# Kernel optimization log

Measured on AMD Instinct MI355X. Metric: run time of the kernel, lower is better.

Reference implementation:

```python
import jax, jax.numpy as jnp
import numpy as np

N = 8192
IN_F = 128
OUT_F = 64
ALPHA = 0.2  # LeakyReLU negative slope
EDGE_P = 0.02  # adjacency density
NEG_INF = -1e12


def setup_inputs() -> dict:
    key = jax.random.key(0)
    k1, k2, k3, k4 = jax.random.split(key, 4)
    input_h = jax.random.normal(k1, (N, IN_F), dtype=jnp.float32)
    # sparse-ish 0/1 adjacency mask, with self-loops so every softmax row is valid
    adj = (jax.random.uniform(k2, (N, N)) < EDGE_P).astype(jnp.float32)
    adj = adj + jnp.eye(N, dtype=jnp.float32)
    # xavier_uniform with gain 1.414 as in the torch init
    def xavier(k, shape, gain=1.414):
        fan_in, fan_out = shape[0], shape[1]
        bound = gain * np.sqrt(6.0 / (fan_in + fan_out))
        return jax.random.uniform(k, shape, jnp.float32, -bound, bound)
    W = xavier(k3, (IN_F, OUT_F))
    a = xavier(k4, (2 * OUT_F, 1))
    return {"input_h": input_h, "adj": adj, "W": W, "a": a}


def reference(input_h, adj, W, a):
    # Wh: [N, F]
    Wh = input_h @ W
    # e[i, j] = leakyrelu(a1 . Wh_i + a2 . Wh_j)  (decomposed, no N*N*2F concat)
    a1 = a[:OUT_F, 0]   # [F]
    a2 = a[OUT_F:, 0]   # [F]
    s_src = Wh @ a1     # [N]
    s_dst = Wh @ a2     # [N]
    e = jax.nn.leaky_relu(s_src[:, None] + s_dst[None, :], negative_slope=ALPHA)  # [N, N]
    att = jnp.where(adj > 0, e, NEG_INF)
    att = jax.nn.softmax(att, axis=1)
    # dropout is identity in eval mode (training=False)
    out_h = att @ Wh    # [N, F]
    return out_h
```

## Files before the change

### kernel.cpp

```cpp
#include <hip/hip_runtime.h>
#include <hip/hip_bf16.h>

#define N 8192
#define IN_F 128
#define OUT_F 64
#define ALPHA 0.2f
#define LOG2E 1.442695040888963f

typedef __attribute__((ext_vector_type(8))) short short8;
typedef __attribute__((ext_vector_type(4))) float f32x4;

__device__ __forceinline__ float cvt(float x) { return x; }
__device__ __forceinline__ float cvt(__hip_bfloat16 x) { return __bfloat162float(x); }

__device__ __forceinline__ bool probe_fp32(const void* adj) {
    unsigned int u = *(const unsigned int*)adj;
    return (u == 0x3F800000u) || (u == 0x40000000u);
}

__device__ __forceinline__ short f2bf(float x) {
    union { __hip_bfloat16 b; short s; } u;
    u.b = __float2bfloat16(x);
    return u.s;
}
__device__ __forceinline__ float bfbits2f(short s) {
    union { unsigned int u; float f; } v;
    v.u = ((unsigned int)(unsigned short)s) << 16;
    return v.f;
}

template <typename T>
__device__ __forceinline__ void k1_body(
    const T* __restrict__ h, const T* __restrict__ W, const T* __restrict__ a,
    unsigned short* __restrict__ WhT, float* __restrict__ s_src, float* __restrict__ s_dst,
    float (*WfT)[132], float (*hrow)[IN_F])
{
    const int tid  = threadIdx.x;
    const int w    = tid >> 6;
    const int lane = tid & 63;
    const int R0   = blockIdx.x * 16;

    for (int idx = tid; idx < IN_F * OUT_F; idx += 256) {
        int t = idx >> 6, f = idx & 63;
        WfT[f][t] = cvt(W[idx]);
    }
    for (int idx = tid; idx < 16 * IN_F; idx += 256) {
        int r = idx >> 7, c = idx & 127;
        hrow[r][c] = cvt(h[(size_t)(R0 + r) * IN_F + c]);
    }
    __syncthreads();

    const float a1 = cvt(a[lane]);
    const float a2 = cvt(a[OUT_F + lane]);

    for (int rr = 0; rr < 4; ++rr) {
        const int rloc = w * 4 + rr;
        const int i    = R0 + rloc;
        float acc = 0.f;
        #pragma unroll 8
        for (int b = 0; b < 32; ++b) {
            const float4 wv = *(const float4*)&WfT[lane][b * 4];
            const float4 hv = *(const float4*)&hrow[rloc][b * 4];
            acc = fmaf(hv.x, wv.x, acc);
            acc = fmaf(hv.y, wv.y, acc);
            acc = fmaf(hv.z, wv.z, acc);
            acc = fmaf(hv.w, wv.w, acc);
        }
        WhT[(size_t)lane * N + i] = (unsigned short)f2bf(acc);

        float s1 = acc * a1, s2 = acc * a2;
        #pragma unroll
        for (int off = 32; off; off >>= 1) {
            s1 += __shfl_xor(s1, off, 64);
            s2 += __shfl_xor(s2, off, 64);
        }
        if (lane == 0) { s_src[i] = s1; s_dst[i] = s2; }
    }
}

__global__ __launch_bounds__(256) void gat_k1(
    const void* h, const void* W, const void* a, const void* adj,
    unsigned short* WhT, float* s_src, float* s_dst)
{
    __shared__ float WfT[OUT_F][132];
    __shared__ float hrow[16][IN_F];
    if (probe_fp32(adj))
        k1_body<float>((const float*)h, (const float*)W, (const float*)a,
                       WhT, s_src, s_dst, WfT, hrow);
    else
        k1_body<__hip_bfloat16>((const __hip_bfloat16*)h, (const __hip_bfloat16*)W,
                                (const __hip_bfloat16*)a, WhT, s_src, s_dst, WfT, hrow);
}

#define K2_WAVES 8
template <typename TADJ, bool OUT_F32>
__device__ __forceinline__ void k2_body(
    const TADJ* __restrict__ adj,
    const unsigned short* __restrict__ WhT,
    const float* __restrict__ s_src,
    const float* __restrict__ s_dst,
    void* __restrict__ outv,
    float (*Cpart)[16][65], float (*Lpart)[16])
{
    const int tid  = threadIdx.x;
    const int wave = tid >> 6;
    const int lane = tid & 63;
    const int quad = lane >> 4;
    const int l15  = lane & 15;
    const int R0   = blockIdx.x * 16;

    const int   row = R0 + l15;
    const float si  = s_src[row];
    const TADJ* __restrict__ arow = adj + (size_t)row * N;

    f32x4 acc[4];
    #pragma unroll
    for (int nt = 0; nt < 4; ++nt) acc[nt] = (f32x4)0.f;
    float ls = 0.f;

    const int jw = wave * 1024;

    for (int kt = 0; kt < 32; ++kt) {
        const int jq = jw + kt * 32 + quad * 8;

        unsigned int bits[8];
        if constexpr (sizeof(TADJ) == 4) {
            const uint4 b0 = *(const uint4*)(arow + jq);
            const uint4 b1 = *(const uint4*)(arow + jq + 4);
            bits[0] = b0.x; bits[1] = b0.y; bits[2] = b0.z; bits[3] = b0.w;
            bits[4] = b1.x; bits[5] = b1.y; bits[6] = b1.z; bits[7] = b1.w;
        } else {
            const uint4 a8 = *(const uint4*)(arow + jq);
            bits[0] = a8.x & 0xffffu; bits[1] = a8.x >> 16;
            bits[2] = a8.y & 0xffffu; bits[3] = a8.y >> 16;
            bits[4] = a8.z & 0xffffu; bits[5] = a8.z >> 16;
            bits[6] = a8.w & 0xffffu; bits[7] = a8.w >> 16;
        }

        const float4 sd0 = *(const float4*)(s_dst + jq);
        const float4 sd1 = *(const float4*)(s_dst + jq + 4);

        short8 bfr[4];
        #pragma unroll
        for (int nt = 0; nt < 4; ++nt)
            bfr[nt] = *(const short8*)(WhT + (size_t)(nt * 16 + l15) * N + jq);

        const float sdv[8] = {sd0.x, sd0.y, sd0.z, sd0.w, sd1.x, sd1.y, sd1.z, sd1.w};

        short8 A;
        #pragma unroll
        for (int t = 0; t < 8; ++t) {
            float e = si + sdv[t];
            e = fmaxf(e, ALPHA * e);
            float p = (bits[t] != 0u) ? __builtin_exp2f(e * LOG2E) : 0.f;
            A[t] = f2bf(p);
            ls += bfbits2f(A[t]);
        }

        #pragma unroll
        for (int nt = 0; nt < 4; ++nt)
            acc[nt] = __builtin_amdgcn_mfma_f32_16x16x32_bf16(A, bfr[nt], acc[nt], 0, 0, 0);
    }

    ls += __shfl_xor(ls, 16, 64);
    ls += __shfl_xor(ls, 32, 64);
    if (quad == 0) Lpart[wave][l15] = ls;

    #pragma unroll
    for (int nt = 0; nt < 4; ++nt)
        #pragma unroll
        for (int reg = 0; reg < 4; ++reg)
            Cpart[wave][quad * 4 + reg][nt * 16 + l15] = acc[nt][reg];

    __syncthreads();

    for (int idx = tid; idx < 16 * OUT_F; idx += 512) {
        const int i = idx >> 6, f = idx & 63;
        float s = 0.f, l = 0.f;
        #pragma unroll
        for (int w = 0; w < K2_WAVES; ++w) {
            s += Cpart[w][i][f];
            l += Lpart[w][i];
        }
        const float v = s / l;
        if constexpr (OUT_F32)
            ((float*)outv)[(size_t)(R0 + i) * OUT_F + f] = v;
        else
            ((__hip_bfloat16*)outv)[(size_t)(R0 + i) * OUT_F + f] = __float2bfloat16(v);
    }
}

__global__ __launch_bounds__(512) void gat_k2(
    const void* adj, const unsigned short* WhT,
    const float* s_src, const float* s_dst, void* out)
{
    __shared__ float Cpart[K2_WAVES][16][65];
    __shared__ float Lpart[K2_WAVES][16];
    if (probe_fp32(adj))
        k2_body<float, true>((const float*)adj, WhT, s_src, s_dst, out, Cpart, Lpart);
    else
        k2_body<unsigned short, false>((const unsigned short*)adj, WhT, s_src, s_dst,
                                       out, Cpart, Lpart);
}

extern "C" void kernel_launch(void* const* d_in, const int* in_sizes, int n_in,
                              void* d_out, int out_size, void* d_ws, size_t ws_size,
                              hipStream_t stream) {
    const void* h   = d_in[0];
    const void* adj = d_in[1];
    const void* W   = d_in[2];
    const void* a   = d_in[3];

    char* ws = (char*)d_ws;
    unsigned short* WhT = (unsigned short*)ws;
    float* s_src = (float*)(ws + (size_t)OUT_F * N * 2);
    float* s_dst = s_src + N;

    gat_k1<<<N / 16, 256, 0, stream>>>(h, W, a, adj, WhT, s_src, s_dst);
    gat_k2<<<N / 16, 512, 0, stream>>>(adj, WhT, s_src, s_dst, d_out);
}
```

Measured before the change: 434.8 us.

## Store Wh in MFMA fragment-major layout and keep W column in registers

Kernel 1 now writes the bf16 Wh matrix in a tiled layout matching the B-operand fragments of the 16x16x32 MFMA, so each wave in kernel 2 reads one contiguous 1 KB block per n-tile instead of 16 strided rows. Kernel 1 also drops the shared-memory transposed copy of W and holds each lane's W column in 128 registers. The aim is coalesced B-fragment loads in the main attention kernel. The cost is higher register pressure in kernel 1 and scattered 2-byte stores when writing the tiled layout.

```diff
diff --git a/kernel.cpp b/kernel.cpp
--- a/kernel.cpp
+++ b/kernel.cpp
@@ -32,18 +32,19 @@
 template <typename T>
 __device__ __forceinline__ void k1_body(
     const T* __restrict__ h, const T* __restrict__ W, const T* __restrict__ a,
-    unsigned short* __restrict__ WhT, float* __restrict__ s_src, float* __restrict__ s_dst,
-    float (*WfT)[132], float (*hrow)[IN_F])
+    unsigned short* __restrict__ WhF, float* __restrict__ s_src, float* __restrict__ s_dst,
+    float (*hrow)[IN_F])
 {
     const int tid  = threadIdx.x;
     const int w    = tid >> 6;
     const int lane = tid & 63;
     const int R0   = blockIdx.x * 16;
 
-    for (int idx = tid; idx < IN_F * OUT_F; idx += 256) {
-        int t = idx >> 6, f = idx & 63;
-        WfT[f][t] = cvt(W[idx]);
-    }
+    float Wcol[IN_F];
+    #pragma unroll
+    for (int t = 0; t < IN_F; ++t)
+        Wcol[t] = cvt(W[t * OUT_F + lane]);
+
     for (int idx = tid; idx < 16 * IN_F; idx += 256) {
         int r = idx >> 7, c = idx & 127;
         hrow[r][c] = cvt(h[(size_t)(R0 + r) * IN_F + c]);
@@ -52,21 +53,22 @@
 
     const float a1 = cvt(a[lane]);
     const float a2 = cvt(a[OUT_F + lane]);
+    const int nt = lane >> 4, l15 = lane & 15;
 
     for (int rr = 0; rr < 4; ++rr) {
         const int rloc = w * 4 + rr;
-        const int i    = R0 + rloc;
+        const int j    = R0 + rloc;
         float acc = 0.f;
-        #pragma unroll 8
+        #pragma unroll
         for (int b = 0; b < 32; ++b) {
-            const float4 wv = *(const float4*)&WfT[lane][b * 4];
             const float4 hv = *(const float4*)&hrow[rloc][b * 4];
-            acc = fmaf(hv.x, wv.x, acc);
-            acc = fmaf(hv.y, wv.y, acc);
-            acc = fmaf(hv.z, wv.z, acc);
-            acc = fmaf(hv.w, wv.w, acc);
-        }
-        WhT[(size_t)lane * N + i] = (unsigned short)f2bf(acc);
+            acc = fmaf(hv.x, Wcol[b * 4 + 0], acc);
+            acc = fmaf(hv.y, Wcol[b * 4 + 1], acc);
+            acc = fmaf(hv.z, Wcol[b * 4 + 2], acc);
+            acc = fmaf(hv.w, Wcol[b * 4 + 3], acc);
+        }
+        WhF[((size_t)(j >> 5) * 4 + nt) * 512 + ((j >> 3) & 3) * 128 + l15 * 8 + (j & 7)]
+            = (unsigned short)f2bf(acc);
 
         float s1 = acc * a1, s2 = acc * a2;
         #pragma unroll
@@ -74,29 +76,28 @@
             s1 += __shfl_xor(s1, off, 64);
             s2 += __shfl_xor(s2, off, 64);
         }
-        if (lane == 0) { s_src[i] = s1; s_dst[i] = s2; }
+        if (lane == 0) { s_src[j] = s1; s_dst[j] = s2; }
     }
 }
 
 __global__ __launch_bounds__(256) void gat_k1(
     const void* h, const void* W, const void* a, const void* adj,
-    unsigned short* WhT, float* s_src, float* s_dst)
-{
-    __shared__ float WfT[OUT_F][132];
+    unsigned short* WhF, float* s_src, float* s_dst)
+{
     __shared__ float hrow[16][IN_F];
     if (probe_fp32(adj))
         k1_body<float>((const float*)h, (const float*)W, (const float*)a,
-                       WhT, s_src, s_dst, WfT, hrow);
+                       WhF, s_src, s_dst, hrow);
     else
         k1_body<__hip_bfloat16>((const __hip_bfloat16*)h, (const __hip_bfloat16*)W,
-                                (const __hip_bfloat16*)a, WhT, s_src, s_dst, WfT, hrow);
+                                (const __hip_bfloat16*)a, WhF, s_src, s_dst, hrow);
 }
 
 #define K2_WAVES 8
 template <typename TADJ, bool OUT_F32>
 __device__ __forceinline__ void k2_body(
     const TADJ* __restrict__ adj,
-    const unsigned short* __restrict__ WhT,
+    const unsigned short* __restrict__ WhF,
     const float* __restrict__ s_src,
     const float* __restrict__ s_dst,
     void* __restrict__ outv,
@@ -140,10 +141,11 @@
         const float4 sd0 = *(const float4*)(s_dst + jq);
         const float4 sd1 = *(const float4*)(s_dst + jq + 4);
 
+        const unsigned short* tb = WhF + (size_t)(wave * 32 + kt) * 2048;
         short8 bfr[4];
         #pragma unroll
         for (int nt = 0; nt < 4; ++nt)
-            bfr[nt] = *(const short8*)(WhT + (size_t)(nt * 16 + l15) * N + jq);
+            bfr[nt] = *(const short8*)(tb + nt * 512 + lane * 8);
 
         const float sdv[8] = {sd0.x, sd0.y, sd0.z, sd0.w, sd1.x, sd1.y, sd1.z, sd1.w};
 
@@ -191,15 +193,15 @@
 }
 
 __global__ __launch_bounds__(512) void gat_k2(
-    const void* adj, const unsigned short* WhT,
+    const void* adj, const unsigned short* WhF,
     const float* s_src, const float* s_dst, void* out)
 {
     __shared__ float Cpart[K2_WAVES][16][65];
     __shared__ float Lpart[K2_WAVES][16];
     if (probe_fp32(adj))
-        k2_body<float, true>((const float*)adj, WhT, s_src, s_dst, out, Cpart, Lpart);
+        k2_body<float, true>((const float*)adj, WhF, s_src, s_dst, out, Cpart, Lpart);
     else
-        k2_body<unsigned short, false>((const unsigned short*)adj, WhT, s_src, s_dst,
+        k2_body<unsigned short, false>((const unsigned short*)adj, WhF, s_src, s_dst,
                                        out, Cpart, Lpart);
 }
 
@@ -212,10 +214,10 @@
     const void* a   = d_in[3];
 
     char* ws = (char*)d_ws;
-    unsigned short* WhT = (unsigned short*)ws;
+    unsigned short* WhF = (unsigned short*)ws;
     float* s_src = (float*)(ws + (size_t)OUT_F * N * 2);
     float* s_dst = s_src + N;
 
-    gat_k1<<<N / 16, 256, 0, stream>>>(h, W, a, adj, WhT, s_src, s_dst);
-    gat_k2<<<N / 16, 512, 0, stream>>>(adj, WhT, s_src, s_dst, d_out);
-}
+    gat_k1<<<N / 16, 256, 0, stream>>>(h, W, a, adj, WhF, s_src, s_dst);
+    gat_k2<<<N / 16, 512, 0, stream>>>(adj, WhF, s_src, s_dst, d_out);
+}
```

Measured after the change: 416.2 us. -4.3%, faster.
